# Optimization experiments

Hardware: AMD Instinct MI355X
Metric: run time of the kernel (lower is better)

Reference implementation:

```python
import jax, jax.numpy as jnp
import numpy as np

B, S, D, H, DK, DV = 4, 1024, 1024, 16, 64, 64
NEG = jnp.float32(-1e10)


def setup_inputs() -> dict:
    key = jax.random.key(0)
    ks = jax.random.split(key, 9)
    q = jax.random.normal(ks[0], (B, S, D), dtype=jnp.float32)
    k = jax.random.normal(ks[1], (B, S, D), dtype=jnp.float32)
    v = jax.random.normal(ks[2], (B, S, D), dtype=jnp.float32)
    pad_mask_1 = jax.random.randint(ks[3], (B,), 1, S + 1, dtype=jnp.int32)
    pad_mask_2 = jax.random.randint(ks[4], (B,), 1, S + 1, dtype=jnp.int32)
    # Per-head projection weights stacked over heads (torch Linear, bias=False).
    sc = 1.0 / np.sqrt(D)
    Wq = jax.random.uniform(ks[5], (H, D, DK), jnp.float32, -sc, sc)
    Wk = jax.random.uniform(ks[6], (H, D, DK), jnp.float32, -sc, sc)
    Wv = jax.random.uniform(ks[7], (H, D, DV), jnp.float32, -sc, sc)
    Wo = jax.random.uniform(ks[8], (H * DV, D), jnp.float32, -sc, sc)
    return {"q": q, "k": k, "v": v, "pad_mask_1": pad_mask_1,
            "pad_mask_2": pad_mask_2, "Wq": Wq, "Wk": Wk, "Wv": Wv, "Wo": Wo}


def reference(q, k, v, pad_mask_1, pad_mask_2, Wq, Wk, Wv, Wo):
    Bq, Sq, _ = q.shape
    scale = jnp.sqrt(jnp.float32(Wq.shape[-1]))
    qh = jnp.einsum('bsd,hdk->bhsk', q, Wq)   # [B,H,S,DK]
    kh = jnp.einsum('bsd,hdk->bhsk', k, Wk)
    vh = jnp.einsum('bsd,hdv->bhsv', v, Wv)
    w = jnp.einsum('bhqk,bhtk->bhqt', qh, kh) / scale  # [B,H,S,S]
    idx = jnp.arange(Sq)
    # pad_mask_1: mask key columns >= length; pad_mask_2: mask query rows >= length
    key_dead = idx[None, :] >= pad_mask_1[:, None]      # [B,S]
    row_dead = idx[None, :] >= pad_mask_2[:, None]      # [B,S]
    w = jnp.where(key_dead[:, None, None, :], NEG, w)
    w = jnp.where(row_dead[:, None, :, None], NEG, w)
    # causal: w.tril() + (-1e10).triu(1) == keep lower triangle, NEG strictly above
    causal = idx[None, :] > idx[:, None]                # [S,S] strictly upper
    w = jnp.where(causal[None, None], NEG, w)
    a = jax.nn.softmax(w, axis=-1)
    o = jnp.einsum('bhqt,bhtv->bhqv', a, vh)            # [B,H,S,DV]
    o = o.transpose(0, 2, 1, 3).reshape(Bq, Sq, -1)     # concat heads (head-major)
    return o @ Wo
```

## Files before the change

kernel.cpp:

```cpp
#include <hip/hip_runtime.h>

#define B_ 4
#define S_ 1024
#define D_ 1024
#define H_ 16
#define BSD (B_*S_*D_)

typedef unsigned short ushort_t;
typedef __attribute__((ext_vector_type(8))) __bf16 bf16x8;
typedef __attribute__((ext_vector_type(8))) ushort_t ushortx8;
typedef __attribute__((ext_vector_type(4))) float f32x4;

__device__ __forceinline__ ushort_t f2bf(float f) {
  union { float f; unsigned int u; } x; x.f = f;
  unsigned int r = x.u + 0x7fffu + ((x.u >> 16) & 1u);
  return (ushort_t)(r >> 16);
}

__device__ __forceinline__ void gll16(const void* g, void* l) {
  __builtin_amdgcn_global_load_lds(
      (const __attribute__((address_space(1))) unsigned int*)g,
      (__attribute__((address_space(3))) unsigned int*)l, 16, 0, 0);
}

#define PBAR() do { asm volatile("s_waitcnt lgkmcnt(0)" ::: "memory"); \
                    __builtin_amdgcn_s_barrier(); \
                    asm volatile("" ::: "memory"); } while (0)

__global__ __launch_bounds__(256) void transpose_w(
    const float* __restrict__ Wq, const float* __restrict__ Wk,
    const float* __restrict__ Wv, const float* __restrict__ Wo,
    ushort_t* __restrict__ WqT, ushort_t* __restrict__ WkT,
    ushort_t* __restrict__ WvT, ushort_t* __restrict__ WoT)
{
  __shared__ float tile[64][65];
  int blk = blockIdx.x;
  const float* src; ushort_t* dst;
  size_t sbase, dbase; int ld_src, ld_dst, r0, c0;
  if (blk < 768) {
    int tz = blk / 256;
    int rem = blk % 256; int head = rem >> 4; int kt = rem & 15;
    src = (tz == 0) ? Wq : (tz == 1) ? Wk : Wv;
    dst = (tz == 0) ? WqT : (tz == 1) ? WkT : WvT;
    sbase = (size_t)head * 1024 * 64; dbase = (size_t)head * 64 * 1024;
    ld_src = 64; ld_dst = 1024; r0 = kt * 64; c0 = 0;
  } else {
    int idx = blk - 768; src = Wo; dst = WoT;
    sbase = 0; dbase = 0; ld_src = 1024; ld_dst = 1024;
    r0 = (idx >> 4) * 64; c0 = (idx & 15) * 64;
  }
  int tid = threadIdx.x; int col = tid & 63; int rbase = tid >> 6;
  #pragma unroll
  for (int j = 0; j < 16; ++j) {
    int row = j * 4 + rbase;
    tile[row][col] = src[sbase + (size_t)(r0 + row) * ld_src + c0 + col];
  }
  __syncthreads();
  #pragma unroll
  for (int j = 0; j < 16; ++j) {
    int orow = j * 4 + rbase;
    dst[dbase + (size_t)(c0 + orow) * ld_dst + r0 + col] = f2bf(tile[col][orow]);
  }
}

__device__ __forceinline__ void gemm_pipe_f32A(
    const float* __restrict__ Af, const ushort_t* __restrict__ BT,
    ushort_t* __restrict__ Cb, int epi, int m0, int n0, int K)
{
  __shared__ __align__(16) ushort_t As[2][128 * 64];
  __shared__ __align__(16) ushort_t Bs[2][128 * 64];
  const int tid = threadIdx.x;
  const int wave = tid >> 6, lane = tid & 63;
  const int wm = wave >> 2, wn = wave & 3;

  f32x4 acc[4][2] = {};
  float4   ra0[2][2], ra1[2][2];
  ushortx8 rb0[2],    rb1[2];

  int offs[2], gofs[2];
  #pragma unroll
  for (int i = 0; i < 2; ++i) {
    int off = ((i * 8 + wave) << 10) + lane * 16;
    int row = off >> 7, cb = off & 127;
    int lcb = cb ^ ((row & 7) << 4);
    offs[i] = off;
    gofs[i] = row * K + (lcb >> 1);
  }

  auto loadAB = [&](float4 (&ar)[2][2], ushortx8 (&br)[2], int k0) {
    #pragma unroll
    for (int i = 0; i < 2; ++i) {
      const float* asrc = Af + (size_t)m0 * K + gofs[i] + k0;
      ar[i][0] = *(const float4*)(asrc);
      ar[i][1] = *(const float4*)(asrc + 4);
      br[i] = *(const ushortx8*)(BT + (size_t)n0 * K + gofs[i] + k0);
    }
  };
  auto writeAB = [&](int buf, const float4 (&ar)[2][2], const ushortx8 (&br)[2]) {
    #pragma unroll
    for (int i = 0; i < 2; ++i) {
      ushortx8 tv;
      #pragma unroll
      for (int j = 0; j < 4; ++j) {
        tv[j]     = f2bf(((const float*)&ar[i][0])[j]);
        tv[4 + j] = f2bf(((const float*)&ar[i][1])[j]);
      }
      *(ushortx8*)((char*)As[buf] + offs[i]) = tv;
      *(ushortx8*)((char*)Bs[buf] + offs[i]) = br[i];
    }
  };
  auto compute = [&](int buf) {
    #pragma unroll
    for (int kk = 0; kk < 2; ++kk) {
      bf16x8 af[4], bfr[2];
      #pragma unroll
      for (int mf = 0; mf < 4; ++mf) {
        int row = wm * 64 + mf * 16 + (lane & 15);
        int cb = kk * 64 + ((lane >> 4) << 4);
        af[mf] = *(const bf16x8*)((const char*)As[buf] + (row << 7) + (cb ^ ((row & 7) << 4)));
      }
      #pragma unroll
      for (int nf = 0; nf < 2; ++nf) {
        int row = wn * 32 + nf * 16 + (lane & 15);
        int cb = kk * 64 + ((lane >> 4) << 4);
        bfr[nf] = *(const bf16x8*)((const char*)Bs[buf] + (row << 7) + (cb ^ ((row & 7) << 4)));
      }
      #pragma unroll
      for (int mf = 0; mf < 4; ++mf)
        #pragma unroll
        for (int nf = 0; nf < 2; ++nf)
          acc[mf][nf] = __builtin_amdgcn_mfma_f32_16x16x32_bf16(af[mf], bfr[nf], acc[mf][nf], 0, 0, 0);
    }
  };

  const int nt = K >> 6;
  loadAB(ra0, rb0, 0);
  writeAB(0, ra0, rb0);
  loadAB(ra1, rb1, 64);
  PBAR();

  for (int t = 0; t < nt - 3; t += 2) {
    loadAB(ra0, rb0, (t + 2) << 6);
    __builtin_amdgcn_sched_barrier(0);
    compute(0);
    writeAB(1, ra1, rb1);
    PBAR();
    loadAB(ra1, rb1, (t + 3) << 6);
    __builtin_amdgcn_sched_barrier(0);
    compute(1);
    writeAB(0, ra0, rb0);
    PBAR();
  }
  compute(0);
  writeAB(1, ra1, rb1);
  PBAR();
  compute(1);

  #pragma unroll
  for (int mf = 0; mf < 4; ++mf) {
    #pragma unroll
    for (int nf = 0; nf < 2; ++nf) {
      #pragma unroll
      for (int r = 0; r < 4; ++r) {
        int m = m0 + wm * 64 + mf * 16 + ((lane >> 4) << 2) + r;
        int n = n0 + wn * 32 + nf * 16 + (lane & 15);
        float val = acc[mf][nf][r];
        if (epi == 0) {
          int b = m >> 10, s = m & 1023, h = n >> 6, dk = n & 63;
          Cb[((((size_t)(b * H_ + h)) << 10) + s) * 64 + dk] = f2bf(val);
        } else {
          int b = m >> 10, s = m & 1023, h = n >> 6, dv = n & 63;
          Cb[((((size_t)(b * H_ + h)) * 64 + dv) << 10) + s] = f2bf(val);
        }
      }
    }
  }
}

__device__ __forceinline__ void gemm_pipe_bf16(
    const ushort_t* __restrict__ A, const ushort_t* __restrict__ BT,
    float* __restrict__ Cf, int m0, int n0, int K)
{
  __shared__ __align__(16) ushort_t As[2][128 * 64];
  __shared__ __align__(16) ushort_t Bs[2][128 * 64];
  const int tid = threadIdx.x;
  const int wave = tid >> 6, lane = tid & 63;
  const int wm = wave >> 2, wn = wave & 3;

  f32x4 acc[4][2] = {};
  ushortx8 ra0[2], ra1[2], rb0[2], rb1[2];

  int offs[2], gofs[2];
  #pragma unroll
  for (int i = 0; i < 2; ++i) {
    int off = ((i * 8 + wave) << 10) + lane * 16;
    int row = off >> 7, cb = off & 127;
    int lcb = cb ^ ((row & 7) << 4);
    offs[i] = off;
    gofs[i] = row * K + (lcb >> 1);
  }

  auto loadAB = [&](ushortx8 (&ar)[2], ushortx8 (&br)[2], int k0) {
    #pragma unroll
    for (int i = 0; i < 2; ++i) {
      ar[i] = *(const ushortx8*)(A  + (size_t)m0 * K + gofs[i] + k0);
      br[i] = *(const ushortx8*)(BT + (size_t)n0 * K + gofs[i] + k0);
    }
  };
  auto writeAB = [&](int buf, const ushortx8 (&ar)[2], const ushortx8 (&br)[2]) {
    #pragma unroll
    for (int i = 0; i < 2; ++i) {
      *(ushortx8*)((char*)As[buf] + offs[i]) = ar[i];
      *(ushortx8*)((char*)Bs[buf] + offs[i]) = br[i];
    }
  };
  auto compute = [&](int buf) {
    #pragma unroll
    for (int kk = 0; kk < 2; ++kk) {
      bf16x8 af[4], bfr[2];
      #pragma unroll
      for (int mf = 0; mf < 4; ++mf) {
        int row = wm * 64 + mf * 16 + (lane & 15);
        int cb = kk * 64 + ((lane >> 4) << 4);
        af[mf] = *(const bf16x8*)((const char*)As[buf] + (row << 7) + (cb ^ ((row & 7) << 4)));
      }
      #pragma unroll
      for (int nf = 0; nf < 2; ++nf) {
        int row = wn * 32 + nf * 16 + (lane & 15);
        int cb = kk * 64 + ((lane >> 4) << 4);
        bfr[nf] = *(const bf16x8*)((const char*)Bs[buf] + (row << 7) + (cb ^ ((row & 7) << 4)));
      }
      #pragma unroll
      for (int mf = 0; mf < 4; ++mf)
        #pragma unroll
        for (int nf = 0; nf < 2; ++nf)
          acc[mf][nf] = __builtin_amdgcn_mfma_f32_16x16x32_bf16(af[mf], bfr[nf], acc[mf][nf], 0, 0, 0);
    }
  };

  const int nt = K >> 6;
  loadAB(ra0, rb0, 0);
  writeAB(0, ra0, rb0);
  loadAB(ra1, rb1, 64);
  PBAR();

  for (int t = 0; t < nt - 3; t += 2) {
    loadAB(ra0, rb0, (t + 2) << 6);
    __builtin_amdgcn_sched_barrier(0);
    compute(0);
    writeAB(1, ra1, rb1);
    PBAR();
    loadAB(ra1, rb1, (t + 3) << 6);
    __builtin_amdgcn_sched_barrier(0);
    compute(1);
    writeAB(0, ra0, rb0);
    PBAR();
  }
  compute(0);
  writeAB(1, ra1, rb1);
  PBAR();
  compute(1);

  #pragma unroll
  for (int mf = 0; mf < 4; ++mf) {
    #pragma unroll
    for (int nf = 0; nf < 2; ++nf) {
      #pragma unroll
      for (int r = 0; r < 4; ++r) {
        int m = m0 + wm * 64 + mf * 16 + ((lane >> 4) << 2) + r;
        int n = n0 + wn * 32 + nf * 16 + (lane & 15);
        Cf[(size_t)m * 1024 + n] = acc[mf][nf][r];
      }
    }
  }
}

__global__ __launch_bounds__(512, 4) void proj_gemm(
    const float* q, const float* k, const float* v,
    const ushort_t* WqT, const ushort_t* WkT, const ushort_t* WvT,
    const int* __restrict__ pad1p, const int* __restrict__ pad2p,
    ushort_t* qh, ushort_t* kh, ushort_t* vhT)
{
  int f = blockIdx.x;
  int c = ((f >> 6) << 3) | (f & 7);
  int y = (f >> 3) & 7;
  int z = c >> 5, x = c & 31;
  if (z < 2) {
    int b = x >> 3;
    int s0 = (x & 7) << 7;
    int lim = (z == 0) ? pad2p[b] : pad1p[b];
    if (s0 >= lim) return;
  }
  const float* A = (z == 0) ? q : (z == 1) ? k : v;
  const ushort_t* BT = (z == 0) ? WqT : (z == 1) ? WkT : WvT;
  ushort_t* C = (z == 0) ? qh : (z == 1) ? kh : vhT;
  gemm_pipe_f32A(A, BT, C, (z == 2) ? 1 : 0, x * 128, y * 128, 1024);
}

__global__ __launch_bounds__(512, 4) void out_gemm(
    const ushort_t* o, const ushort_t* WoT, float* out)
{
  int f = blockIdx.x;
  int xcd = f & 7;
  int slot = f >> 3;
  int x = xcd * 4 + (slot >> 3);
  int y = slot & 7;
  gemm_pipe_bf16(o, WoT, out, x * 128, y * 128, 1024);
}

__global__ __launch_bounds__(256) void meanv_kernel(
    const ushort_t* __restrict__ vhT, float* __restrict__ meanV)
{
  int row = blockIdx.x * 4 + (threadIdx.x >> 6);
  int lane = threadIdx.x & 63;
  const ushort_t* src = vhT + ((size_t)row << 10) + lane * 16;
  float s = 0.f;
  #pragma unroll
  for (int i = 0; i < 2; ++i) {
    bf16x8 v = *(const bf16x8*)(src + i * 8);
    #pragma unroll
    for (int j = 0; j < 8; ++j) s += (float)v[j];
  }
  #pragma unroll
  for (int mm = 1; mm < 64; mm <<= 1) s += __shfl_xor(s, mm);
  if (lane == 0) meanV[row] = s * (1.0f / 1024.0f);
}

__global__ __launch_bounds__(256) void attn_kernel(
    const ushort_t* __restrict__ qh, const ushort_t* __restrict__ kh,
    const ushort_t* __restrict__ vhT, const float* __restrict__ meanV,
    const int* __restrict__ pad1p, const int* __restrict__ pad2p,
    ushort_t* __restrict__ o)
{
  const int bh = blockIdx.x;
  const int b = bh >> 4, h = bh & 15;
  const int q0 = blockIdx.y << 6;
  const int pad1 = pad1p[b], pad2 = pad2p[b];
  const int tid = threadIdx.x, wave = tid >> 6, lane = tid & 63;

  if (q0 >= pad2) {
    int dv = tid & 63;
    int rw = tid >> 6;
    ushort_t mb = f2bf(meanV[(bh << 6) + dv]);
    for (int r = rw; r < 64; r += 4)
      o[(((size_t)((b << 10) + q0 + r)) << 10) + (h << 6) + dv] = mb;
    return;
  }

  __shared__ __align__(16) ushort_t Ks[64 * 64];
  __shared__ __align__(16) ushort_t Vs[64 * 64];
  __shared__ __align__(16) ushort_t Ps[4][16 * 64];

  const ushort_t* qbase = qh + ((size_t)bh << 16);
  const ushort_t* kbase = kh + ((size_t)bh << 16);
  const ushort_t* vbase = vhT + ((size_t)bh << 16);

  const int qrow = q0 + wave * 16 + (lane & 15);
  bf16x8 qf[2];
  qf[0] = *(const bf16x8*)(qbase + (size_t)qrow * 64 + ((lane >> 4) << 3));
  qf[1] = *(const bf16x8*)(qbase + (size_t)qrow * 64 + 32 + ((lane >> 4) << 3));

  f32x4 acc[4] = {};
  float mrow[4] = { -1e30f, -1e30f, -1e30f, -1e30f };
  float lrow[4] = { 0.f, 0.f, 0.f, 0.f };
  const int ribase = q0 + wave * 16 + ((lane >> 4) << 2);

  int t_hi = min(q0 + 63, min(pad2 - 1, pad1 - 1));
  int nb = (t_hi >> 6) + 1;

  for (int kb = 0; kb < nb; ++kb) {
    const int t0 = kb << 6;
    #pragma unroll
    for (int i = 0; i < 2; ++i) {
      int off = ((i * 4 + wave) << 10) + lane * 16;
      int row = off >> 7;
      int cb = off & 127;
      int lcb = cb ^ ((row & 7) << 4);
      gll16(kbase + (size_t)(t0 + row) * 64 + (lcb >> 1), (char*)Ks + off);
      gll16(vbase + ((size_t)row << 10) + t0 + (lcb >> 1), (char*)Vs + off);
    }
    __syncthreads();

    f32x4 sc[4];
    #pragma unroll
    for (int nf = 0; nf < 4; ++nf) {
      sc[nf] = (f32x4){0.f, 0.f, 0.f, 0.f};
      #pragma unroll
      for (int kk = 0; kk < 2; ++kk) {
        int trow = nf * 16 + (lane & 15);
        int cb = kk * 64 + ((lane >> 4) << 4);
        bf16x8 kf = *(const bf16x8*)((const char*)Ks + (trow << 7) + (cb ^ ((trow & 7) << 4)));
        sc[nf] = __builtin_amdgcn_mfma_f32_16x16x32_bf16(qf[kk], kf, sc[nf], 0, 0, 0);
      }
    }

    float pv[4][4];
    #pragma unroll
    for (int r = 0; r < 4; ++r) {
      const int irow = ribase + r;
      float sval[4];
      float rmax = -1e30f;
      #pragma unroll
      for (int nf = 0; nf < 4; ++nf) {
        int t = t0 + nf * 16 + (lane & 15);
        float vv = sc[nf][r] * 0.125f;
        if (t > irow || t >= pad1) vv = -1e10f;
        sval[nf] = vv;
        rmax = fmaxf(rmax, vv);
      }
      #pragma unroll
      for (int mm = 1; mm < 16; mm <<= 1) rmax = fmaxf(rmax, __shfl_xor(rmax, mm));
      float nm = fmaxf(mrow[r], rmax);
      float fscale = __expf(mrow[r] - nm);
      float rsum = 0.f;
      #pragma unroll
      for (int nf = 0; nf < 4; ++nf) {
        float p = __expf(sval[nf] - nm);
        pv[nf][r] = p;
        rsum += p;
      }
      #pragma unroll
      for (int mm = 1; mm < 16; mm <<= 1) rsum += __shfl_xor(rsum, mm);
      mrow[r] = nm;
      lrow[r] = lrow[r] * fscale + rsum;
      #pragma unroll
      for (int dvf = 0; dvf < 4; ++dvf) acc[dvf][r] *= fscale;
    }

    #pragma unroll
    for (int nf = 0; nf < 4; ++nf) {
      #pragma unroll
      for (int r = 0; r < 4; ++r) {
        int prow = ((lane >> 4) << 2) + r;
        int cbw = (nf * 16 + (lane & 15)) * 2;
        *(ushort_t*)((char*)Ps[wave] + (prow << 7) + (cbw ^ ((prow & 7) << 4))) = f2bf(pv[nf][r]);
      }
    }

    #pragma unroll
    for (int kk = 0; kk < 2; ++kk) {
      int prow = lane & 15;
      int cb = kk * 64 + ((lane >> 4) << 4);
      bf16x8 pf = *(const bf16x8*)((const char*)Ps[wave] + (prow << 7) + (cb ^ ((prow & 7) << 4)));
      #pragma unroll
      for (int dvf = 0; dvf < 4; ++dvf) {
        int vrow = dvf * 16 + (lane & 15);
        bf16x8 vfr = *(const bf16x8*)((const char*)Vs + (vrow << 7) + (cb ^ ((vrow & 7) << 4)));
        acc[dvf] = __builtin_amdgcn_mfma_f32_16x16x32_bf16(pf, vfr, acc[dvf], 0, 0, 0);
      }
    }
    __syncthreads();
  }

  #pragma unroll
  for (int dvf = 0; dvf < 4; ++dvf) {
    #pragma unroll
    for (int r = 0; r < 4; ++r) {
      int irow = ribase + r;
      int dv = dvf * 16 + (lane & 15);
      float val;
      if (irow < pad2) val = acc[dvf][r] * (1.0f / lrow[r]);
      else val = meanV[(bh << 6) + dv];
      o[(((size_t)((b << 10) + irow)) << 10) + (h << 6) + dv] = f2bf(val);
    }
  }
}

extern "C" void kernel_launch(void* const* d_in, const int* in_sizes, int n_in,
                              void* d_out, int out_size, void* d_ws, size_t ws_size,
                              hipStream_t stream) {
  (void)in_sizes; (void)n_in; (void)out_size; (void)ws_size;
  const float* q = (const float*)d_in[0];
  const float* k = (const float*)d_in[1];
  const float* v = (const float*)d_in[2];
  const int* pad1 = (const int*)d_in[3];
  const int* pad2 = (const int*)d_in[4];
  const float* Wq = (const float*)d_in[5];
  const float* Wk = (const float*)d_in[6];
  const float* Wv = (const float*)d_in[7];
  const float* Wo = (const float*)d_in[8];
  float* out = (float*)d_out;

  char* ws = (char*)d_ws;
  const size_t MB = 1u << 20;
  ushort_t* WqT = (ushort_t*)(ws + 24 * MB);
  ushort_t* WkT = (ushort_t*)(ws + 26 * MB);
  ushort_t* WvT = (ushort_t*)(ws + 28 * MB);
  ushort_t* WoT = (ushort_t*)(ws + 30 * MB);
  ushort_t* qh  = (ushort_t*)(ws + 32 * MB);
  ushort_t* kh  = (ushort_t*)(ws + 40 * MB);
  ushort_t* vhT = (ushort_t*)(ws + 48 * MB);
  ushort_t* ob  = (ushort_t*)(ws + 56 * MB);
  float* meanV  = (float*)(ws + 64 * MB);

  transpose_w<<<1024, 256, 0, stream>>>(Wq, Wk, Wv, Wo, WqT, WkT, WvT, WoT);
  proj_gemm<<<768, 512, 0, stream>>>(q, k, v, WqT, WkT, WvT, pad1, pad2, qh, kh, vhT);
  meanv_kernel<<<1024, 256, 0, stream>>>(vhT, meanV);
  attn_kernel<<<dim3(64, 16), 256, 0, stream>>>(qh, kh, vhT, meanV, pad1, pad2, ob);
  out_gemm<<<256, 512, 0, stream>>>(ob, WoT, out);
}
```

Before: 93.12 us.

## Pre-convert q/k/v to bf16 and stage projection GEMM tiles via global_load_lds

Adds a separate kernel that converts q, k and v from fp32 to bf16 into workspace buffers, skipping rows that the padding lengths mark dead for q and k. The projection GEMM then reads bf16 inputs and stages its A/B tiles straight into LDS with global_load_lds, replacing the register round-trip and in-loop conversion with a simpler double-buffered loop. This removes per-tile conversion work and register pressure from the GEMM. In exchange it adds an extra pass that reads fp32 activations and writes bf16 copies, and uses plain __syncthreads without the explicit prefetch schedule.

```diff
diff --git a/kernel.cpp b/kernel.cpp
--- a/kernel.cpp
+++ b/kernel.cpp
@@ -26,6 +26,27 @@
 #define PBAR() do { asm volatile("s_waitcnt lgkmcnt(0)" ::: "memory"); \
                     __builtin_amdgcn_s_barrier(); \
                     asm volatile("" ::: "memory"); } while (0)
+
+__global__ __launch_bounds__(256) void convert_qkv(
+    const float* __restrict__ q, const float* __restrict__ k, const float* __restrict__ v,
+    const int* __restrict__ pad1p, const int* __restrict__ pad2p,
+    ushort_t* __restrict__ qb, ushort_t* __restrict__ kb, ushort_t* __restrict__ vb)
+{
+  int z = blockIdx.y;
+  int row = blockIdx.x;
+  if (z < 2) {
+    int b = row >> 10, s = row & 1023;
+    int lim = (z == 0) ? pad2p[b] : pad1p[b];
+    if (s >= lim) return;
+  }
+  const float* src = (z == 0) ? q : (z == 1) ? k : v;
+  ushort_t* dst = (z == 0) ? qb : (z == 1) ? kb : vb;
+  int idx = (row << 10) + threadIdx.x * 4;
+  float4 f = *(const float4*)(src + idx);
+  ushort4 r;
+  r.x = f2bf(f.x); r.y = f2bf(f.y); r.z = f2bf(f.z); r.w = f2bf(f.w);
+  *(ushort4*)(dst + idx) = r;
+}
 
 __global__ __launch_bounds__(256) void transpose_w(
     const float* __restrict__ Wq, const float* __restrict__ Wk,
@@ -63,8 +84,8 @@
   }
 }
 
-__device__ __forceinline__ void gemm_pipe_f32A(
-    const float* __restrict__ Af, const ushort_t* __restrict__ BT,
+__device__ __forceinline__ void gemm_gll(
+    const ushort_t* __restrict__ A, const ushort_t* __restrict__ BT,
     ushort_t* __restrict__ Cb, int epi, int m0, int n0, int K)
 {
   __shared__ __align__(16) ushort_t As[2][128 * 64];
@@ -74,8 +95,110 @@
   const int wm = wave >> 2, wn = wave & 3;
 
   f32x4 acc[4][2] = {};
-  float4   ra0[2][2], ra1[2][2];
-  ushortx8 rb0[2],    rb1[2];
+
+  auto stage = [&](int buf, int k0) {
+    #pragma unroll
+    for (int i = 0; i < 2; ++i) {
+      int off = ((i * 8 + wave) << 10) + lane * 16;
+      int row = off >> 7;
+      int cb = off & 127;
+      int lcb = cb ^ ((row & 7) << 4);
+      gll16(A + (size_t)(m0 + row) * K + k0 + (lcb >> 1), (char*)As[buf] + off);
+      gll16(BT + (size_t)(n0 + row) * K + k0 + (lcb >> 1), (char*)Bs[buf] + off);
+    }
+  };
+
+  auto compute = [&](int buf) {
+    #pragma unroll
+    for (int kk = 0; kk < 2; ++kk) {
+      bf16x8 af[4], bfr[2];
+      #pragma unroll
+      for (int mf = 0; mf < 4; ++mf) {
+        int row = wm * 64 + mf * 16 + (lane & 15);
+        int cb = kk * 64 + ((lane >> 4) << 4);
+        af[mf] = *(const bf16x8*)((const char*)As[buf] + (row << 7) + (cb ^ ((row & 7) << 4)));
+      }
+      #pragma unroll
+      for (int nf = 0; nf < 2; ++nf) {
+        int row = wn * 32 + nf * 16 + (lane & 15);
+        int cb = kk * 64 + ((lane >> 4) << 4);
+        bfr[nf] = *(const bf16x8*)((const char*)Bs[buf] + (row << 7) + (cb ^ ((row & 7) << 4)));
+      }
+      #pragma unroll
+      for (int mf = 0; mf < 4; ++mf)
+        #pragma unroll
+        for (int nf = 0; nf < 2; ++nf)
+          acc[mf][nf] = __builtin_amdgcn_mfma_f32_16x16x32_bf16(af[mf], bfr[nf], acc[mf][nf], 0, 0, 0);
+    }
+  };
+
+  const int nt = K >> 6;
+  stage(0, 0);
+  __syncthreads();
+  int cur = 0;
+  for (int t = 0; t < nt - 1; ++t) {
+    stage(cur ^ 1, (t + 1) << 6);
+    compute(cur);
+    __syncthreads();
+    cur ^= 1;
+  }
+  compute(cur);
+
+  #pragma unroll
+  for (int mf = 0; mf < 4; ++mf) {
+    #pragma unroll
+    for (int nf = 0; nf < 2; ++nf) {
+      #pragma unroll
+      for (int r = 0; r < 4; ++r) {
+        int m = m0 + wm * 64 + mf * 16 + ((lane >> 4) << 2) + r;
+        int n = n0 + wn * 32 + nf * 16 + (lane & 15);
+        float val = acc[mf][nf][r];
+        if (epi == 0) {
+          int b = m >> 10, s = m & 1023, h = n >> 6, dk = n & 63;
+          Cb[((((size_t)(b * H_ + h)) << 10) + s) * 64 + dk] = f2bf(val);
+        } else {
+          int b = m >> 10, s = m & 1023, h = n >> 6, dv = n & 63;
+          Cb[((((size_t)(b * H_ + h)) * 64 + dv) << 10) + s] = f2bf(val);
+        }
+      }
+    }
+  }
+}
+
+__global__ __launch_bounds__(512, 4) void proj_gemm(
+    const ushort_t* qb, const ushort_t* kb, const ushort_t* vb,
+    const ushort_t* WqT, const ushort_t* WkT, const ushort_t* WvT,
+    const int* __restrict__ pad1p, const int* __restrict__ pad2p,
+    ushort_t* qh, ushort_t* kh, ushort_t* vhT)
+{
+  int f = blockIdx.x;
+  int c = ((f >> 6) << 3) | (f & 7);
+  int y = (f >> 3) & 7;
+  int z = c >> 5, x = c & 31;
+  if (z < 2) {
+    int b = x >> 3;
+    int s0 = (x & 7) << 7;
+    int lim = (z == 0) ? pad2p[b] : pad1p[b];
+    if (s0 >= lim) return;
+  }
+  const ushort_t* A = (z == 0) ? qb : (z == 1) ? kb : vb;
+  const ushort_t* BT = (z == 0) ? WqT : (z == 1) ? WkT : WvT;
+  ushort_t* C = (z == 0) ? qh : (z == 1) ? kh : vhT;
+  gemm_gll(A, BT, C, (z == 2) ? 1 : 0, x * 128, y * 128, 1024);
+}
+
+__device__ __forceinline__ void gemm_pipe_bf16(
+    const ushort_t* __restrict__ A, const ushort_t* __restrict__ BT,
+    float* __restrict__ Cf, int m0, int n0, int K)
+{
+  __shared__ __align__(16) ushort_t As[2][128 * 64];
+  __shared__ __align__(16) ushort_t Bs[2][128 * 64];
+  const int tid = threadIdx.x;
+  const int wave = tid >> 6, lane = tid & 63;
+  const int wm = wave >> 2, wn = wave & 3;
+
+  f32x4 acc[4][2] = {};
+  ushortx8 ra0[2], ra1[2], rb0[2], rb1[2];
 
   int offs[2], gofs[2];
   #pragma unroll
@@ -87,25 +210,17 @@
     gofs[i] = row * K + (lcb >> 1);
   }
 
-  auto loadAB = [&](float4 (&ar)[2][2], ushortx8 (&br)[2], int k0) {
+  auto loadAB = [&](ushortx8 (&ar)[2], ushortx8 (&br)[2], int k0) {
     #pragma unroll
     for (int i = 0; i < 2; ++i) {
-      const float* asrc = Af + (size_t)m0 * K + gofs[i] + k0;
-      ar[i][0] = *(const float4*)(asrc);
-      ar[i][1] = *(const float4*)(asrc + 4);
+      ar[i] = *(const ushortx8*)(A  + (size_t)m0 * K + gofs[i] + k0);
       br[i] = *(const ushortx8*)(BT + (size_t)n0 * K + gofs[i] + k0);
     }
   };
-  auto writeAB = [&](int buf, const float4 (&ar)[2][2], const ushortx8 (&br)[2]) {
+  auto writeAB = [&](int buf, const ushortx8 (&ar)[2], const ushortx8 (&br)[2]) {
     #pragma unroll
     for (int i = 0; i < 2; ++i) {
-      ushortx8 tv;
-      #pragma unroll
-      for (int j = 0; j < 4; ++j) {
-        tv[j]     = f2bf(((const float*)&ar[i][0])[j]);
-        tv[4 + j] = f2bf(((const float*)&ar[i][1])[j]);
-      }
-      *(ushortx8*)((char*)As[buf] + offs[i]) = tv;
+      *(ushortx8*)((char*)As[buf] + offs[i]) = ar[i];
       *(ushortx8*)((char*)Bs[buf] + offs[i]) = br[i];
     }
   };
@@ -164,137 +279,10 @@
       for (int r = 0; r < 4; ++r) {
         int m = m0 + wm * 64 + mf * 16 + ((lane >> 4) << 2) + r;
         int n = n0 + wn * 32 + nf * 16 + (lane & 15);
-        float val = acc[mf][nf][r];
-        if (epi == 0) {
-          int b = m >> 10, s = m & 1023, h = n >> 6, dk = n & 63;
-          Cb[((((size_t)(b * H_ + h)) << 10) + s) * 64 + dk] = f2bf(val);
-        } else {
-          int b = m >> 10, s = m & 1023, h = n >> 6, dv = n & 63;
-          Cb[((((size_t)(b * H_ + h)) * 64 + dv) << 10) + s] = f2bf(val);
-        }
-      }
-    }
-  }
-}
-
-__device__ __forceinline__ void gemm_pipe_bf16(
-    const ushort_t* __restrict__ A, const ushort_t* __restrict__ BT,
-    float* __restrict__ Cf, int m0, int n0, int K)
-{
-  __shared__ __align__(16) ushort_t As[2][128 * 64];
-  __shared__ __align__(16) ushort_t Bs[2][128 * 64];
-  const int tid = threadIdx.x;
-  const int wave = tid >> 6, lane = tid & 63;
-  const int wm = wave >> 2, wn = wave & 3;
-
-  f32x4 acc[4][2] = {};
-  ushortx8 ra0[2], ra1[2], rb0[2], rb1[2];
-
-  int offs[2], gofs[2];
-  #pragma unroll
-  for (int i = 0; i < 2; ++i) {
-    int off = ((i * 8 + wave) << 10) + lane * 16;
-    int row = off >> 7, cb = off & 127;
-    int lcb = cb ^ ((row & 7) << 4);
-    offs[i] = off;
-    gofs[i] = row * K + (lcb >> 1);
-  }
-
-  auto loadAB = [&](ushortx8 (&ar)[2], ushortx8 (&br)[2], int k0) {
-    #pragma unroll
-    for (int i = 0; i < 2; ++i) {
-      ar[i] = *(const ushortx8*)(A  + (size_t)m0 * K + gofs[i] + k0);
-      br[i] = *(const ushortx8*)(BT + (size_t)n0 * K + gofs[i] + k0);
-    }
-  };
-  auto writeAB = [&](int buf, const ushortx8 (&ar)[2], const ushortx8 (&br)[2]) {
-    #pragma unroll
-    for (int i = 0; i < 2; ++i) {
-      *(ushortx8*)((char*)As[buf] + offs[i]) = ar[i];
-      *(ushortx8*)((char*)Bs[buf] + offs[i]) = br[i];
-    }
-  };
-  auto compute = [&](int buf) {
-    #pragma unroll
-    for (int kk = 0; kk < 2; ++kk) {
-      bf16x8 af[4], bfr[2];
-      #pragma unroll
-      for (int mf = 0; mf < 4; ++mf) {
-        int row = wm * 64 + mf * 16 + (lane & 15);
-        int cb = kk * 64 + ((lane >> 4) << 4);
-        af[mf] = *(const bf16x8*)((const char*)As[buf] + (row << 7) + (cb ^ ((row & 7) << 4)));
-      }
-      #pragma unroll
-      for (int nf = 0; nf < 2; ++nf) {
-        int row = wn * 32 + nf * 16 + (lane & 15);
-        int cb = kk * 64 + ((lane >> 4) << 4);
-        bfr[nf] = *(const bf16x8*)((const char*)Bs[buf] + (row << 7) + (cb ^ ((row & 7) << 4)));
-      }
-      #pragma unroll
-      for (int mf = 0; mf < 4; ++mf)
-        #pragma unroll
-        for (int nf = 0; nf < 2; ++nf)
-          acc[mf][nf] = __builtin_amdgcn_mfma_f32_16x16x32_bf16(af[mf], bfr[nf], acc[mf][nf], 0, 0, 0);
-    }
-  };
-
-  const int nt = K >> 6;
-  loadAB(ra0, rb0, 0);
-  writeAB(0, ra0, rb0);
-  loadAB(ra1, rb1, 64);
-  PBAR();
-
-  for (int t = 0; t < nt - 3; t += 2) {
-    loadAB(ra0, rb0, (t + 2) << 6);
-    __builtin_amdgcn_sched_barrier(0);
-    compute(0);
-    writeAB(1, ra1, rb1);
-    PBAR();
-    loadAB(ra1, rb1, (t + 3) << 6);
-    __builtin_amdgcn_sched_barrier(0);
-    compute(1);
-    writeAB(0, ra0, rb0);
-    PBAR();
-  }
-  compute(0);
-  writeAB(1, ra1, rb1);
-  PBAR();
-  compute(1);
-
-  #pragma unroll
-  for (int mf = 0; mf < 4; ++mf) {
-    #pragma unroll
-    for (int nf = 0; nf < 2; ++nf) {
-      #pragma unroll
-      for (int r = 0; r < 4; ++r) {
-        int m = m0 + wm * 64 + mf * 16 + ((lane >> 4) << 2) + r;
-        int n = n0 + wn * 32 + nf * 16 + (lane & 15);
         Cf[(size_t)m * 1024 + n] = acc[mf][nf][r];
       }
     }
   }
-}
-
-__global__ __launch_bounds__(512, 4) void proj_gemm(
-    const float* q, const float* k, const float* v,
-    const ushort_t* WqT, const ushort_t* WkT, const ushort_t* WvT,
-    const int* __restrict__ pad1p, const int* __restrict__ pad2p,
-    ushort_t* qh, ushort_t* kh, ushort_t* vhT)
-{
-  int f = blockIdx.x;
-  int c = ((f >> 6) << 3) | (f & 7);
-  int y = (f >> 3) & 7;
-  int z = c >> 5, x = c & 31;
-  if (z < 2) {
-    int b = x >> 3;
-    int s0 = (x & 7) << 7;
-    int lim = (z == 0) ? pad2p[b] : pad1p[b];
-    if (s0 >= lim) return;
-  }
-  const float* A = (z == 0) ? q : (z == 1) ? k : v;
-  const ushort_t* BT = (z == 0) ? WqT : (z == 1) ? WkT : WvT;
-  ushort_t* C = (z == 0) ? qh : (z == 1) ? kh : vhT;
-  gemm_pipe_f32A(A, BT, C, (z == 2) ? 1 : 0, x * 128, y * 128, 1024);
 }
 
 __global__ __launch_bounds__(512, 4) void out_gemm(
@@ -483,6 +471,9 @@
 
   char* ws = (char*)d_ws;
   const size_t MB = 1u << 20;
+  ushort_t* qb  = (ushort_t*)(ws + 0 * MB);
+  ushort_t* kb  = (ushort_t*)(ws + 8 * MB);
+  ushort_t* vb  = (ushort_t*)(ws + 16 * MB);
   ushort_t* WqT = (ushort_t*)(ws + 24 * MB);
   ushort_t* WkT = (ushort_t*)(ws + 26 * MB);
   ushort_t* WvT = (ushort_t*)(ws + 28 * MB);
@@ -493,8 +484,9 @@
   ushort_t* ob  = (ushort_t*)(ws + 56 * MB);
   float* meanV  = (float*)(ws + 64 * MB);
 
+  convert_qkv<<<dim3(4096, 3), 256, 0, stream>>>(q, k, v, pad1, pad2, qb, kb, vb);
   transpose_w<<<1024, 256, 0, stream>>>(Wq, Wk, Wv, Wo, WqT, WkT, WvT, WoT);
-  proj_gemm<<<768, 512, 0, stream>>>(q, k, v, WqT, WkT, WvT, pad1, pad2, qh, kh, vhT);
+  proj_gemm<<<768, 512, 0, stream>>>(qb, kb, vb, WqT, WkT, WvT, pad1, pad2, qh, kh, vhT);
   meanv_kernel<<<1024, 256, 0, stream>>>(vhT, meanV);
   attn_kernel<<<dim3(64, 16), 256, 0, stream>>>(qh, kh, vhT, meanV, pad1, pad2, ob);
   out_gemm<<<256, 512, 0, stream>>>(ob, WoT, out);
```

New measurement: 94.36 us. About the same (+1.3%).
